# Performance work log

Measured on AMD Instinct MI355X. Metric: run time of the kernel, lower is better.

Reference implementation:

```python
import jax, jax.numpy as jnp
import numpy as np

B, N, D, H, K = 4, 256, 128, 8, 16

def setup_inputs() -> dict:
    key = jax.random.key(0)
    ks = jax.random.split(key, 6)
    h = jax.random.normal(ks[0], (B, N, D), jnp.float32)
    e_att = jax.random.normal(ks[1], (B, N, N, H, K), jnp.float32)
    e_val = jax.random.normal(ks[2], (B, N, N, H, K), jnp.float32)
    mask = jnp.ones((B, N), jnp.float32)
    scale = 1.0 / np.sqrt(D).astype(np.float32)
    Wq = jax.random.normal(ks[3], (D, H * K), jnp.float32) * scale
    Wk = jax.random.normal(ks[4], (D, H * K), jnp.float32) * scale
    Wv = jax.random.normal(ks[5], (D, H * K), jnp.float32) * scale
    return {"h": h, "e_att": e_att, "e_val": e_val, "mask": mask, "Wq": Wq, "Wk": Wk, "Wv": Wv}

def reference(h, e_att, e_val, mask, Wq, Wk, Wv):
    b, n, _ = h.shape
    Q = (h @ Wq).reshape(b, n, H, K)
    Kh = (h @ Wk).reshape(b, n, H, K) * (float(K) ** -0.5)
    V = (h @ Wv).reshape(b, n, H, K)
    # (b,i,j,h) dot-product scores, broadcast over k, plus per-edge bias
    scores = jnp.einsum('bihk,bjhk->bijh', Q, Kh)[..., None] + e_att
    scores = jnp.exp(jnp.clip(scores, -5.0, 5.0))
    attn_mask = mask[:, :, None, None, None] * mask[:, None, :, None, None]
    scores = scores * attn_mask
    softmax_denom = jnp.maximum(scores.sum(axis=2), 1e-6)  # (b,i,h,k)
    scores = scores * attn_mask  # dropout p=0 -> identity on mask
    out = jnp.einsum('bijhk,bjhk->bihk', scores, V)
    out = out + (scores * e_val).sum(axis=2)
    out = out / softmax_denom
    return out.reshape(b, n, H * K)
```

## Files before the change

### kernel.cpp

```cpp
#include <hip/hip_runtime.h>
#include <hip/hip_bf16.h>

#define Bb 4
#define Nn 256
#define Dd 128
#define Hh 8
#define Kk 16
#define HK 128
#define BN 1024

__global__ __launch_bounds__(128) void qkv_kernel(
    const float* __restrict__ h,
    const float* __restrict__ Wq,
    const float* __restrict__ Wk,
    const float* __restrict__ Wv,
    float* __restrict__ Qw, float* __restrict__ Kw, float* __restrict__ Vw)
{
    __shared__ float hrows[8][Dd];
    const int rb = blockIdx.x;
    const int t  = threadIdx.x;
    #pragma unroll
    for (int r = 0; r < 8; ++r)
        hrows[r][t] = h[(size_t)(rb * 8 + r) * Dd + t];
    __syncthreads();

    float aq[8], ak[8], av[8];
    #pragma unroll
    for (int r = 0; r < 8; ++r) { aq[r] = 0.f; ak[r] = 0.f; av[r] = 0.f; }

    for (int d = 0; d < Dd; ++d) {
        const float wq = Wq[d * HK + t];
        const float wk = Wk[d * HK + t];
        const float wv = Wv[d * HK + t];
        #pragma unroll
        for (int r = 0; r < 8; ++r) {
            const float hv = hrows[r][d];
            aq[r] = fmaf(hv, wq, aq[r]);
            ak[r] = fmaf(hv, wk, ak[r]);
            av[r] = fmaf(hv, wv, av[r]);
        }
    }
    #pragma unroll
    for (int r = 0; r < 8; ++r) {
        const size_t o = (size_t)(rb * 8 + r) * HK + t;
        Qw[o] = aq[r];
        Kw[o] = ak[r] * 0.25f;
        Vw[o] = av[r];
    }
}

__global__ __launch_bounds__(256) void attn_kernel(
    const float* __restrict__ e_att,
    const float* __restrict__ e_val,
    const float* __restrict__ mask,
    const float* __restrict__ Qw,
    const float* __restrict__ Kw,
    const float* __restrict__ Vw,
    float* __restrict__ out)
{
    __shared__ float qrow[HK];
    __shared__ float mrow[Nn];
    __shared__ float buf[3 * 8 * HK];

    const int t  = threadIdx.x;
    const int bi = blockIdx.x;
    const int b  = bi >> 8;

    if (t < HK) qrow[t] = Qw[(size_t)bi * HK + t];
    mrow[t] = mask[b * Nn + t];
    __syncthreads();

    const float maski = mrow[bi & 255];

    float* qk_s = buf;
    #pragma unroll
    for (int p = 0; p < 8; ++p) {
        const int idx = p * 256 + t;
        const int j   = idx >> 3;
        const int hh  = idx & 7;
        const float* kp = Kw + (size_t)(b * Nn + j) * HK + hh * Kk;
        const float* qp = qrow + hh * Kk;
        float acc = 0.f;
        #pragma unroll
        for (int k = 0; k < Kk; ++k) acc = fmaf(qp[k], kp[k], acc);
        qk_s[idx] = acc;
    }
    __syncthreads();

    const int q32  = t & 31;
    const int joff = t >> 5;
    const int hk4  = q32 * 4;
    const int hh   = q32 >> 2;

    float acc_d[4] = {0,0,0,0}, acc_v[4] = {0,0,0,0}, acc_e[4] = {0,0,0,0};
    const size_t slice = (size_t)bi * (Nn * HK);

    for (int jb = 0; jb < Nn; jb += 8) {
        const int j = jb + joff;
        const size_t eoff = slice + (size_t)j * HK + hk4;
        const float4 ea = *(const float4*)(e_att + eoff);
        const float4 ev = *(const float4*)(e_val + eoff);
        const float4 v4 = *(const float4*)(Vw + (size_t)(b * Nn + j) * HK + hk4);

        const float qk = qk_s[(j << 3) + hh];
        const float m  = maski * mrow[j];
        const float m2 = m * m;

        const float eaf[4] = {ea.x, ea.y, ea.z, ea.w};
        const float evf[4] = {ev.x, ev.y, ev.z, ev.w};
        const float vv[4]  = {v4.x, v4.y, v4.z, v4.w};

        #pragma unroll
        for (int l = 0; l < 4; ++l) {
            float x = qk + eaf[l];
            x = fminf(fmaxf(x, -5.f), 5.f);
            const float e = __expf(x);
            acc_d[l] = fmaf(e, m, acc_d[l]);
            const float s2 = e * m2;
            acc_v[l] = fmaf(s2, vv[l], acc_v[l]);
            acc_e[l] = fmaf(s2, evf[l], acc_e[l]);
        }
    }
    __syncthreads();

    #pragma unroll
    for (int l = 0; l < 4; ++l) {
        buf[0 * 1024 + joff * HK + hk4 + l] = acc_d[l];
        buf[1 * 1024 + joff * HK + hk4 + l] = acc_v[l];
        buf[2 * 1024 + joff * HK + hk4 + l] = acc_e[l];
    }
    __syncthreads();

    if (t < HK) {
        float D = 0.f, OV = 0.f, OE = 0.f;
        #pragma unroll
        for (int p = 0; p < 8; ++p) {
            D  += buf[0 * 1024 + p * HK + t];
            OV += buf[1 * 1024 + p * HK + t];
            OE += buf[2 * 1024 + p * HK + t];
        }
        out[(size_t)bi * HK + t] = (OV + OE) / fmaxf(D, 1e-6f);
    }
}

extern "C" void kernel_launch(void* const* d_in, const int* in_sizes, int n_in,
                              void* d_out, int out_size, void* d_ws, size_t ws_size,
                              hipStream_t stream) {
    const float* h     = (const float*)d_in[0];
    const float* e_att = (const float*)d_in[1];
    const float* e_val = (const float*)d_in[2];
    const float* mask  = (const float*)d_in[3];
    const float* Wq    = (const float*)d_in[4];
    const float* Wk    = (const float*)d_in[5];
    const float* Wv    = (const float*)d_in[6];
    float* out = (float*)d_out;

    float* Qw = (float*)d_ws;
    float* Kw = Qw + (size_t)BN * HK;
    float* Vw = Kw + (size_t)BN * HK;

    qkv_kernel<<<128, 128, 0, stream>>>(h, Wq, Wk, Wv, Qw, Kw, Vw);
    attn_kernel<<<BN, 256, 0, stream>>>(e_att, e_val, mask, Qw, Kw, Vw, out);
}
```

Baseline: 74.05 us.

## Split QK scores into separate kernel and widen attention blocks to 512 threads

```diff
diff --git a/kernel.cpp b/kernel.cpp
--- a/kernel.cpp
+++ b/kernel.cpp
@@ -49,43 +49,61 @@
     }
 }
 
-__global__ __launch_bounds__(256) void attn_kernel(
+__global__ __launch_bounds__(256) void qk_kernel(
+    const float* __restrict__ Qw,
+    const float* __restrict__ Kw,
+    float* __restrict__ qkg)
+{
+    __shared__ float qrow[HK];
+    const int t  = threadIdx.x;
+    const int bi = blockIdx.x;
+    const int b  = bi >> 8;
+
+    if (t < HK) qrow[t] = Qw[(size_t)bi * HK + t];
+    __syncthreads();
+
+    #pragma unroll
+    for (int p = 0; p < 8; ++p) {
+        const int idx = p * 256 + t;
+        const int j   = idx >> 3;
+        const int hh  = idx & 7;
+        const float4* kp = (const float4*)(Kw + (size_t)(b * Nn + j) * HK + hh * Kk);
+        const float4 k0 = kp[0], k1 = kp[1], k2 = kp[2], k3 = kp[3];
+        const float* qp = qrow + hh * Kk;
+        float acc = 0.f;
+        acc = fmaf(qp[0],  k0.x, acc); acc = fmaf(qp[1],  k0.y, acc);
+        acc = fmaf(qp[2],  k0.z, acc); acc = fmaf(qp[3],  k0.w, acc);
+        acc = fmaf(qp[4],  k1.x, acc); acc = fmaf(qp[5],  k1.y, acc);
+        acc = fmaf(qp[6],  k1.z, acc); acc = fmaf(qp[7],  k1.w, acc);
+        acc = fmaf(qp[8],  k2.x, acc); acc = fmaf(qp[9],  k2.y, acc);
+        acc = fmaf(qp[10], k2.z, acc); acc = fmaf(qp[11], k2.w, acc);
+        acc = fmaf(qp[12], k3.x, acc); acc = fmaf(qp[13], k3.y, acc);
+        acc = fmaf(qp[14], k3.z, acc); acc = fmaf(qp[15], k3.w, acc);
+        qkg[(size_t)bi * 2048 + idx] = acc;
+    }
+}
+
+__global__ __launch_bounds__(512) void attn_kernel(
     const float* __restrict__ e_att,
     const float* __restrict__ e_val,
     const float* __restrict__ mask,
-    const float* __restrict__ Qw,
-    const float* __restrict__ Kw,
+    const float* __restrict__ qkg,
     const float* __restrict__ Vw,
     float* __restrict__ out)
 {
-    __shared__ float qrow[HK];
+    __shared__ float qk_s[2048];
     __shared__ float mrow[Nn];
-    __shared__ float buf[3 * 8 * HK];
+    __shared__ float red[3 * 16 * HK];
 
     const int t  = threadIdx.x;
     const int bi = blockIdx.x;
     const int b  = bi >> 8;
 
-    if (t < HK) qrow[t] = Qw[(size_t)bi * HK + t];
-    mrow[t] = mask[b * Nn + t];
+    ((float4*)qk_s)[t] = ((const float4*)(qkg + (size_t)bi * 2048))[t];
+    if (t < Nn) mrow[t] = mask[b * Nn + t];
     __syncthreads();
 
     const float maski = mrow[bi & 255];
-
-    float* qk_s = buf;
-    #pragma unroll
-    for (int p = 0; p < 8; ++p) {
-        const int idx = p * 256 + t;
-        const int j   = idx >> 3;
-        const int hh  = idx & 7;
-        const float* kp = Kw + (size_t)(b * Nn + j) * HK + hh * Kk;
-        const float* qp = qrow + hh * Kk;
-        float acc = 0.f;
-        #pragma unroll
-        for (int k = 0; k < Kk; ++k) acc = fmaf(qp[k], kp[k], acc);
-        qk_s[idx] = acc;
-    }
-    __syncthreads();
 
     const int q32  = t & 31;
     const int joff = t >> 5;
@@ -95,7 +113,8 @@
     float acc_d[4] = {0,0,0,0}, acc_v[4] = {0,0,0,0}, acc_e[4] = {0,0,0,0};
     const size_t slice = (size_t)bi * (Nn * HK);
 
-    for (int jb = 0; jb < Nn; jb += 8) {
+    #pragma unroll 4
+    for (int jb = 0; jb < Nn; jb += 16) {
         const int j = jb + joff;
         const size_t eoff = slice + (size_t)j * HK + hk4;
         const float4 ea = *(const float4*)(e_att + eoff);
@@ -125,19 +144,19 @@
 
     #pragma unroll
     for (int l = 0; l < 4; ++l) {
-        buf[0 * 1024 + joff * HK + hk4 + l] = acc_d[l];
-        buf[1 * 1024 + joff * HK + hk4 + l] = acc_v[l];
-        buf[2 * 1024 + joff * HK + hk4 + l] = acc_e[l];
+        red[0 * 2048 + joff * HK + hk4 + l] = acc_d[l];
+        red[1 * 2048 + joff * HK + hk4 + l] = acc_v[l];
+        red[2 * 2048 + joff * HK + hk4 + l] = acc_e[l];
     }
     __syncthreads();
 
     if (t < HK) {
         float D = 0.f, OV = 0.f, OE = 0.f;
         #pragma unroll
-        for (int p = 0; p < 8; ++p) {
-            D  += buf[0 * 1024 + p * HK + t];
-            OV += buf[1 * 1024 + p * HK + t];
-            OE += buf[2 * 1024 + p * HK + t];
+        for (int p = 0; p < 16; ++p) {
+            D  += red[0 * 2048 + p * HK + t];
+            OV += red[1 * 2048 + p * HK + t];
+            OE += red[2 * 2048 + p * HK + t];
         }
         out[(size_t)bi * HK + t] = (OV + OE) / fmaxf(D, 1e-6f);
     }
@@ -155,10 +174,12 @@
     const float* Wv    = (const float*)d_in[6];
     float* out = (float*)d_out;
 
-    float* Qw = (float*)d_ws;
-    float* Kw = Qw + (size_t)BN * HK;
-    float* Vw = Kw + (size_t)BN * HK;
+    float* Qw  = (float*)d_ws;
+    float* Kw  = Qw + (size_t)BN * HK;
+    float* Vw  = Kw + (size_t)BN * HK;
+    float* qkg = Vw + (size_t)BN * HK;
 
     qkv_kernel<<<128, 128, 0, stream>>>(h, Wq, Wk, Wv, Qw, Kw, Vw);
-    attn_kernel<<<BN, 256, 0, stream>>>(e_att, e_val, mask, Qw, Kw, Vw, out);
+    qk_kernel<<<BN, 256, 0, stream>>>(Qw, Kw, qkg);
+    attn_kernel<<<BN, 512, 0, stream>>>(e_att, e_val, mask, qkg, Vw, out);
 }
```

Measured after the change: 74.41 us. About the same (+0.5%).
